# Kernel tuning notes

Measured on AMD Instinct MI355X. Metric: run time of the kernel, lower is better.

## Reference

```python
import jax, jax.numpy as jnp
import numpy as np

B = 16384
TEXT_D = 768
TECH_D = 256
IN_D = TEXT_D + TECH_D  # 1024
OUT_D = 1024
E = 8


def setup_inputs() -> dict:
    key = jax.random.key(0)
    ks = jax.random.split(key, 8)
    s_in = 1.0 / np.sqrt(IN_D)
    s_out = 1.0 / np.sqrt(OUT_D)
    return {
        "text_features": jax.random.normal(ks[0], (B, TEXT_D), jnp.float32),
        "technical_features": jax.random.normal(ks[1], (B, TECH_D), jnp.float32),
        # stacked expert params: layer1 [E, IN_D, OUT_D], layer2 [E, OUT_D, OUT_D]
        "W1": jax.random.uniform(ks[2], (E, IN_D, OUT_D), jnp.float32, -s_in, s_in),
        "b1": jax.random.uniform(ks[3], (E, OUT_D), jnp.float32, -s_in, s_in),
        "W2": jax.random.uniform(ks[4], (E, OUT_D, OUT_D), jnp.float32, -s_out, s_out),
        "b2": jax.random.uniform(ks[5], (E, OUT_D), jnp.float32, -s_out, s_out),
        # gating network
        "Wg": jax.random.uniform(ks[6], (IN_D, E), jnp.float32, -s_in, s_in),
        "bg": jax.random.uniform(ks[7], (E,), jnp.float32, -s_in, s_in),
    }


def reference(text_features, technical_features, W1, b1, W2, b2, Wg, bg):
    x = jnp.concatenate([text_features, technical_features], axis=-1)  # [B, IN_D]
    gates = jax.nn.softmax(x @ Wg + bg, axis=-1)                       # [B, E]
    h = jax.nn.relu(jnp.einsum('bi,eio->beo', x, W1) + b1[None])       # [B, E, OUT_D]
    y = jnp.einsum('beo,eop->bep', h, W2) + b2[None]                   # [B, E, OUT_D]
    return jnp.einsum('be,bep->bp', gates, y)                          # [B, OUT_D]
```

## Files before the change

kernel.cpp:

```cpp
#include <hip/hip_runtime.h>
#include <hip/hip_bf16.h>

#define NB 16384
#define TEXT_D 768
#define TECH_D 256
#define IND 1024
#define OUTD 1024
#define NE 8
#define KH2 4096

typedef unsigned short u16;
typedef __bf16 bf16x8 __attribute__((ext_vector_type(8)));
typedef float f32x4 __attribute__((ext_vector_type(4)));

__device__ __forceinline__ u16 f2bf(float f) {
  union { float f; unsigned int u; } x; x.f = f;
  unsigned int u = x.u;
  return (u16)((u + 0x7FFFu + ((u >> 16) & 1u)) >> 16);
}

__device__ __forceinline__ void gload_lds16(const void* g, void* l) {
  __builtin_amdgcn_global_load_lds(
      (const __attribute__((address_space(1))) unsigned int*)g,
      (__attribute__((address_space(3))) unsigned int*)l, 16, 0, 0);
}

__global__ __launch_bounds__(256) void convert_gates(
    const float* __restrict__ text, const float* __restrict__ tech,
    const float* __restrict__ Wg, const float* __restrict__ bg,
    u16* __restrict__ xb, float* __restrict__ gates) {
  int t = threadIdx.x;
  int wave = t >> 6, lane = t & 63;
  int row = blockIdx.x * 4 + wave;

  float acc[NE];
#pragma unroll
  for (int e = 0; e < NE; ++e) acc[e] = 0.f;

#pragma unroll
  for (int j = 0; j < 4; ++j) {
    int col = j * 256 + lane * 4;
    float4 v = (j < 3) ? *(const float4*)&text[(size_t)row * TEXT_D + col]
                       : *(const float4*)&tech[(size_t)row * TECH_D + lane * 4];
    ushort4 o = make_ushort4(f2bf(v.x), f2bf(v.y), f2bf(v.z), f2bf(v.w));
    *(ushort4*)&xb[(size_t)row * IND + col] = o;
    const float* wp = &Wg[(size_t)col * NE];
    float xv[4] = {v.x, v.y, v.z, v.w};
#pragma unroll
    for (int i = 0; i < 4; ++i) {
      float4 w0 = *(const float4*)&wp[i * NE];
      float4 w1 = *(const float4*)&wp[i * NE + 4];
      acc[0] = fmaf(xv[i], w0.x, acc[0]);
      acc[1] = fmaf(xv[i], w0.y, acc[1]);
      acc[2] = fmaf(xv[i], w0.z, acc[2]);
      acc[3] = fmaf(xv[i], w0.w, acc[3]);
      acc[4] = fmaf(xv[i], w1.x, acc[4]);
      acc[5] = fmaf(xv[i], w1.y, acc[5]);
      acc[6] = fmaf(xv[i], w1.z, acc[6]);
      acc[7] = fmaf(xv[i], w1.w, acc[7]);
    }
  }
#pragma unroll
  for (int off = 32; off; off >>= 1)
#pragma unroll
    for (int e = 0; e < NE; ++e) acc[e] += __shfl_xor(acc[e], off);

#pragma unroll
  for (int e = 0; e < NE; ++e) acc[e] += bg[e];
  float mx = acc[0];
#pragma unroll
  for (int e = 1; e < NE; ++e) mx = fmaxf(mx, acc[e]);
  float s = 0.f;
#pragma unroll
  for (int e = 0; e < NE; ++e) { acc[e] = expf(acc[e] - mx); s += acc[e]; }
  float inv = 1.f / s;
  if (lane < NE) gates[(size_t)row * NE + lane] = acc[lane] * inv;
}

__global__ __launch_bounds__(256) void transpose_w12(
    const float* __restrict__ W1, const float* __restrict__ W2,
    u16* __restrict__ W1t, u16* __restrict__ W2t) {
  __shared__ u16 tile[64][65];
  int bid = blockIdx.x;
  int half = bid >> 11;
  int b2 = bid & 2047;
  int e = b2 >> 8;
  int tb = b2 & 255;
  int r0 = (tb >> 4) * 64;
  int c0 = (tb & 15) * 64;
  const float* We; u16* Wte; int ostride;
  if (half == 0) {
    We = W1 + (size_t)e * IND * OUTD;
    Wte = W1t + ((size_t)e << 20);
    ostride = 1024;
  } else {
    We = W2 + (size_t)e * IND * OUTD;
    Wte = W2t + ((size_t)(e >> 2) << 22) + (size_t)(e & 3) * 1024;
    ostride = KH2;
  }
  int t = threadIdx.x;
  int tr = t >> 4;
  int tc = (t & 15) * 4;
#pragma unroll
  for (int j = 0; j < 4; ++j) {
    int row = j * 16 + tr;
    float4 v = *(const float4*)&We[(size_t)(r0 + row) * OUTD + c0 + tc];
    tile[row][tc + 0] = f2bf(v.x);
    tile[row][tc + 1] = f2bf(v.y);
    tile[row][tc + 2] = f2bf(v.z);
    tile[row][tc + 3] = f2bf(v.w);
  }
  __syncthreads();
#pragma unroll
  for (int j = 0; j < 4; ++j) {
    int row = j * 16 + tr;
    ushort4 o = make_ushort4(tile[tc + 0][row], tile[tc + 1][row],
                             tile[tc + 2][row], tile[tc + 3][row]);
    *(ushort4*)&Wte[(size_t)(c0 + row) * ostride + r0 + tc] = o;
  }
}

#define BAR() asm volatile("s_barrier" ::: "memory")
#define VM4() asm volatile("s_waitcnt vmcnt(4)" ::: "memory")

template <int SLOT, int K>
__device__ __forceinline__ void stage_slot(
    const u16* __restrict__ pA, const u16* __restrict__ pB, char* sb, int k0,
    int ch0, int rsub, int koff, int lbyte) {
#pragma unroll
  for (int j = 0; j < 2; ++j) {
    int ch = ch0 + j;
    int r;
    if constexpr (SLOT == 0)      r = (ch >> 3) * 128 + (ch & 7) * 8 + rsub;
    else if constexpr (SLOT == 3) r = 64 + (ch >> 3) * 128 + (ch & 7) * 8 + rsub;
    else if constexpr (SLOT == 1) r = (ch >> 2) * 64 + (ch & 3) * 8 + rsub;
    else                          r = (ch >> 2) * 64 + 32 + (ch & 3) * 8 + rsub;
    const u16* g = (SLOT == 0 || SLOT == 3) ? pA : pB;
    char* lb = sb + ((SLOT == 0 || SLOT == 3) ? 0 : 32768) + r * 128 + lbyte;
    gload_lds16(g + (size_t)r * K + k0 + koff, lb);
  }
}

template <int QH>
__device__ __forceinline__ void load_a(const char* rb, int wr, int lr, int hi,
                                       int swr, bf16x8 (&a)[4][2]) {
#pragma unroll
  for (int i = 0; i < 4; ++i)
#pragma unroll
    for (int ks = 0; ks < 2; ++ks)
      a[i][ks] = *(const bf16x8*)(rb + (wr * 128 + QH * 64 + i * 16 + lr) * 128
                                  + ((ks * 64 + hi * 16) ^ swr));
}

template <int NH>
__device__ __forceinline__ void load_b(const char* rb, int wc, int lr, int hi,
                                       int swr, bf16x8 (&b)[2][2]) {
#pragma unroll
  for (int q = 0; q < 2; ++q)
#pragma unroll
    for (int ks = 0; ks < 2; ++ks)
      b[q][ks] = *(const bf16x8*)(rb + 32768 +
                                  (wc * 64 + (NH * 2 + q) * 16 + lr) * 128
                                  + ((ks * 64 + hi * 16) ^ swr));
}

template <int MH, int NH>
__device__ __forceinline__ void mfma_quad(const bf16x8 (&a)[4][2],
                                          const bf16x8 (&b)[2][2],
                                          f32x4 (&acc)[8][4]) {
  __builtin_amdgcn_s_setprio(1);
#pragma unroll
  for (int i = 0; i < 4; ++i)
#pragma unroll
    for (int q = 0; q < 2; ++q) {
      acc[MH*4+i][NH*2+q] = __builtin_amdgcn_mfma_f32_16x16x32_bf16(
          a[i][0], b[q][0], acc[MH*4+i][NH*2+q], 0, 0, 0);
      acc[MH*4+i][NH*2+q] = __builtin_amdgcn_mfma_f32_16x16x32_bf16(
          a[i][1], b[q][1], acc[MH*4+i][NH*2+q], 0, 0, 0);
    }
  __builtin_amdgcn_s_setprio(0);
}

template <int RB, int K, bool LAST>
__device__ __forceinline__ void ktile(
    const u16* __restrict__ pA, const u16* __restrict__ pB, char* lds, int k0s,
    int ch0, int rsub, int koff, int lbyte,
    int wr, int wc, int lr, int hi, int swr,
    bf16x8 (&a)[4][2], bf16x8 (&b0)[2][2], bf16x8 (&b1)[2][2],
    f32x4 (&acc)[8][4]) {
  const char* rb = lds + RB * 65536;
  char* sb = lds + (RB ^ 1) * 65536;
  load_a<0>(rb, wr, lr, hi, swr, a);
  load_b<0>(rb, wc, lr, hi, swr, b0);
  if constexpr (!LAST) { stage_slot<0, K>(pA, pB, sb, k0s, ch0, rsub, koff, lbyte); VM4(); }
  else                 { asm volatile("s_waitcnt vmcnt(2)" ::: "memory"); }
  BAR();
  mfma_quad<0, 0>(a, b0, acc);
  BAR();
  load_b<1>(rb, wc, lr, hi, swr, b1);
  if constexpr (!LAST) { stage_slot<1, K>(pA, pB, sb, k0s, ch0, rsub, koff, lbyte); VM4(); }
  else                 { asm volatile("s_waitcnt vmcnt(0)" ::: "memory"); }
  BAR();
  mfma_quad<0, 1>(a, b1, acc);
  BAR();
  load_a<1>(rb, wr, lr, hi, swr, a);
  if constexpr (!LAST) { stage_slot<2, K>(pA, pB, sb, k0s, ch0, rsub, koff, lbyte); VM4(); }
  BAR();
  mfma_quad<1, 0>(a, b0, acc);
  BAR();
  if constexpr (!LAST) { stage_slot<3, K>(pA, pB, sb, k0s, ch0, rsub, koff, lbyte); VM4(); }
  BAR();
  mfma_quad<1, 1>(a, b1, acc);
  BAR();
}

template <int K>
__device__ __forceinline__ void core256(const u16* __restrict__ pA,
                                        const u16* __restrict__ pB,
                                        char* lds, int t, f32x4 (&acc)[8][4]) {
  constexpr int KT = K / 64;
  const int l = t & 63;
  const int w = t >> 6;
  const int wr = w >> 2, wc = w & 3;
  const int lr = l & 15, hi = l >> 4;
  const int rsub = l >> 3;
  const int koff = ((l & 7) ^ rsub) << 3;
  const int lbyte = (l & 7) * 16;
  const int ch0 = w * 2;
  const int swr = (lr & 7) << 4;

  bf16x8 a[4][2], b0[2][2], b1[2][2];

  stage_slot<0, K>(pA, pB, lds, 0, ch0, rsub, koff, lbyte);
  stage_slot<1, K>(pA, pB, lds, 0, ch0, rsub, koff, lbyte);
  stage_slot<2, K>(pA, pB, lds, 0, ch0, rsub, koff, lbyte);
  stage_slot<3, K>(pA, pB, lds, 0, ch0, rsub, koff, lbyte);
  VM4(); BAR();

  for (int T = 0; T < KT - 2; T += 2) {
    ktile<0, K, false>(pA, pB, lds, (T + 1) * 64, ch0, rsub, koff, lbyte,
                       wr, wc, lr, hi, swr, a, b0, b1, acc);
    ktile<1, K, false>(pA, pB, lds, (T + 2) * 64, ch0, rsub, koff, lbyte,
                       wr, wc, lr, hi, swr, a, b0, b1, acc);
  }
  ktile<0, K, false>(pA, pB, lds, (KT - 1) * 64, ch0, rsub, koff, lbyte,
                     wr, wc, lr, hi, swr, a, b0, b1, acc);
  ktile<1, K, true>(pA, pB, lds, 0, ch0, rsub, koff, lbyte,
                    wr, wc, lr, hi, swr, a, b0, b1, acc);
  asm volatile("s_waitcnt vmcnt(0)" ::: "memory");
}

__global__ __launch_bounds__(512, 2) void gemm1(
    const u16* __restrict__ xb, const u16* __restrict__ W1t,
    const float* __restrict__ b1, const float* __restrict__ gates,
    u16* __restrict__ Hg, int eg0) {
  __shared__ char lds[131072];
  int t = threadIdx.x;
  int nwg = gridDim.x, cpx = nwg >> 3, bid = blockIdx.x;
  int swz = (bid & 7) * cpx + (bid >> 3);
  int nb = swz & 3, ee = (swz >> 2) & 3, mb = swz >> 4;
  int e = eg0 + ee;

  f32x4 acc[8][4] = {};
  core256<1024>(xb + (size_t)mb * 256 * 1024,
                W1t + ((size_t)e << 20) + (size_t)nb * 256 * 1024,
                lds, t, acc);

  int l = t & 63, w = t >> 6, wr = w >> 2, wc = w & 3, lr = l & 15, hi = l >> 4;
  int m0 = mb * 256 + wr * 128 + hi * 4;
  int n0 = nb * 256 + wc * 64 + lr;
  const float* b1e = b1 + e * OUTD;
#pragma unroll
  for (int m = 0; m < 8; ++m) {
#pragma unroll
    for (int r = 0; r < 4; ++r) {
      int row = m0 + m * 16 + r;
      float g = gates[(size_t)row * NE + e];
#pragma unroll
      for (int nn = 0; nn < 4; ++nn) {
        int n = n0 + nn * 16;
        float v = g * fmaxf(acc[m][nn][r] + b1e[n], 0.f);
        Hg[(size_t)row * KH2 + ee * 1024 + n] = f2bf(v);
      }
    }
  }
}

template <bool FIRST>
__global__ __launch_bounds__(512, 2) void gemm2(
    const u16* __restrict__ Hg, const u16* __restrict__ W2th,
    const float* __restrict__ b2h, const float* __restrict__ gates,
    float* __restrict__ out, int eg0) {
  __shared__ char lds[131072];
  int t = threadIdx.x;
  int nwg = gridDim.x, cpx = nwg >> 3, bid = blockIdx.x;
  int swz = (bid & 7) * cpx + (bid >> 3);
  int nb = swz & 3, mb = swz >> 2;

  f32x4 acc[8][4] = {};
  core256<KH2>(Hg + (size_t)mb * 256 * KH2, W2th + (size_t)nb * 256 * KH2,
               lds, t, acc);

  int l = t & 63, w = t >> 6, wr = w >> 2, wc = w & 3, lr = l & 15, hi = l >> 4;
  int m0 = mb * 256 + wr * 128 + hi * 4;
  int n0 = nb * 256 + wc * 64 + lr;

  float bcol[4][4];
#pragma unroll
  for (int nn = 0; nn < 4; ++nn)
#pragma unroll
    for (int j = 0; j < 4; ++j)
      bcol[nn][j] = b2h[j * OUTD + n0 + nn * 16];

#pragma unroll
  for (int m = 0; m < 8; ++m) {
#pragma unroll
    for (int r = 0; r < 4; ++r) {
      int row = m0 + m * 16 + r;
      float4 ga = *(const float4*)&gates[(size_t)row * NE + eg0];
#pragma unroll
      for (int nn = 0; nn < 4; ++nn) {
        float bias = ga.x * bcol[nn][0] + ga.y * bcol[nn][1] +
                     ga.z * bcol[nn][2] + ga.w * bcol[nn][3];
        size_t oi = (size_t)row * OUTD + n0 + nn * 16;
        float v = acc[m][nn][r] + bias;
        if (FIRST) out[oi] = v;
        else       out[oi] += v;
      }
    }
  }
}

extern "C" void kernel_launch(void* const* d_in, const int* in_sizes, int n_in,
                              void* d_out, int out_size, void* d_ws, size_t ws_size,
                              hipStream_t stream) {
  (void)in_sizes; (void)n_in; (void)out_size; (void)ws_size;
  const float* text = (const float*)d_in[0];
  const float* tech = (const float*)d_in[1];
  const float* W1   = (const float*)d_in[2];
  const float* b1   = (const float*)d_in[3];
  const float* W2   = (const float*)d_in[4];
  const float* b2   = (const float*)d_in[5];
  const float* Wg   = (const float*)d_in[6];
  const float* bg   = (const float*)d_in[7];
  float* out = (float*)d_out;

  char* p = (char*)d_ws;
  u16* xb  = (u16*)p;  p += (size_t)NB * IND * 2;
  u16* W1t = (u16*)p;  p += (size_t)NE * IND * OUTD * 2;
  u16* W2t = (u16*)p;  p += (size_t)NE * OUTD * OUTD * 2;
  float* gates = (float*)p; p += (size_t)NB * NE * 4;
  u16* Hg  = (u16*)p;

  convert_gates<<<dim3(NB / 4), dim3(256), 0, stream>>>(text, tech, Wg, bg, xb, gates);
  transpose_w12<<<dim3(4096), dim3(256), 0, stream>>>(W1, W2, W1t, W2t);

  for (int h = 0; h < 2; ++h) {
    int eg0 = h * 4;
    gemm1<<<dim3(1024), dim3(512), 0, stream>>>(xb, W1t, b1, gates, Hg, eg0);
    const u16* W2th = W2t + ((size_t)h << 22);
    const float* b2h = b2 + (size_t)eg0 * OUTD;
    if (h == 0)
      gemm2<true><<<dim3(256), dim3(512), 0, stream>>>(Hg, W2th, b2h, gates, out, eg0);
    else
      gemm2<false><<<dim3(256), dim3(512), 0, stream>>>(Hg, W2th, b2h, gates, out, eg0);
  }
}
```

Measured before the change: 612.9 us.

## Deepen GEMM K-loop prefetch by staging half-tiles ahead into the current buffer

```diff
diff --git a/kernel.cpp b/kernel.cpp
--- a/kernel.cpp
+++ b/kernel.cpp
@@ -121,7 +121,9 @@
 }
 
 #define BAR() asm volatile("s_barrier" ::: "memory")
+#define VM0() asm volatile("s_waitcnt vmcnt(0)" ::: "memory")
 #define VM4() asm volatile("s_waitcnt vmcnt(4)" ::: "memory")
+#define VM8() asm volatile("s_waitcnt vmcnt(8)" ::: "memory")
 
 template <int SLOT, int K>
 __device__ __forceinline__ void stage_slot(
@@ -181,36 +183,42 @@
   __builtin_amdgcn_s_setprio(0);
 }
 
-template <int RB, int K, bool LAST>
+template <int RB, int K, int MODE>
 __device__ __forceinline__ void ktile(
-    const u16* __restrict__ pA, const u16* __restrict__ pB, char* lds, int k0s,
-    int ch0, int rsub, int koff, int lbyte,
+    const u16* __restrict__ pA, const u16* __restrict__ pB, char* lds,
+    int kH1, int kH0, int ch0, int rsub, int koff, int lbyte,
     int wr, int wc, int lr, int hi, int swr,
     bf16x8 (&a)[4][2], bf16x8 (&b0)[2][2], bf16x8 (&b1)[2][2],
     f32x4 (&acc)[8][4]) {
   const char* rb = lds + RB * 65536;
-  char* sb = lds + (RB ^ 1) * 65536;
+  char* nbuf = lds + (RB ^ 1) * 65536;
+  char* tbuf = lds + RB * 65536;
   load_a<0>(rb, wr, lr, hi, swr, a);
   load_b<0>(rb, wc, lr, hi, swr, b0);
-  if constexpr (!LAST) { stage_slot<0, K>(pA, pB, sb, k0s, ch0, rsub, koff, lbyte); VM4(); }
-  else                 { asm volatile("s_waitcnt vmcnt(2)" ::: "memory"); }
+  if constexpr (MODE < 2) {
+    stage_slot<2, K>(pA, pB, nbuf, kH1, ch0, rsub, koff, lbyte);
+    stage_slot<3, K>(pA, pB, nbuf, kH1, ch0, rsub, koff, lbyte);
+  }
   BAR();
   mfma_quad<0, 0>(a, b0, acc);
+  if constexpr (MODE == 2) { VM0(); } else { VM8(); }
   BAR();
   load_b<1>(rb, wc, lr, hi, swr, b1);
-  if constexpr (!LAST) { stage_slot<1, K>(pA, pB, sb, k0s, ch0, rsub, koff, lbyte); VM4(); }
-  else                 { asm volatile("s_waitcnt vmcnt(0)" ::: "memory"); }
   BAR();
   mfma_quad<0, 1>(a, b1, acc);
   BAR();
   load_a<1>(rb, wr, lr, hi, swr, a);
-  if constexpr (!LAST) { stage_slot<2, K>(pA, pB, sb, k0s, ch0, rsub, koff, lbyte); VM4(); }
   BAR();
   mfma_quad<1, 0>(a, b0, acc);
   BAR();
-  if constexpr (!LAST) { stage_slot<3, K>(pA, pB, sb, k0s, ch0, rsub, koff, lbyte); VM4(); }
+  if constexpr (MODE == 0) {
+    stage_slot<0, K>(pA, pB, tbuf, kH0, ch0, rsub, koff, lbyte);
+    stage_slot<1, K>(pA, pB, tbuf, kH0, ch0, rsub, koff, lbyte);
+  }
   BAR();
   mfma_quad<1, 1>(a, b1, acc);
+  if constexpr (MODE == 0) { VM8(); }
+  else if constexpr (MODE == 1) { VM4(); }
   BAR();
 }
 
@@ -219,6 +227,7 @@
                                         const u16* __restrict__ pB,
                                         char* lds, int t, f32x4 (&acc)[8][4]) {
   constexpr int KT = K / 64;
+  static_assert(KT >= 4 && (KT & 1) == 0, "KT must be even >= 4");
   const int l = t & 63;
   const int w = t >> 6;
   const int wr = w >> 2, wc = w & 3;
@@ -235,19 +244,21 @@
   stage_slot<1, K>(pA, pB, lds, 0, ch0, rsub, koff, lbyte);
   stage_slot<2, K>(pA, pB, lds, 0, ch0, rsub, koff, lbyte);
   stage_slot<3, K>(pA, pB, lds, 0, ch0, rsub, koff, lbyte);
-  VM4(); BAR();
+  stage_slot<0, K>(pA, pB, lds + 65536, 64, ch0, rsub, koff, lbyte);
+  stage_slot<1, K>(pA, pB, lds + 65536, 64, ch0, rsub, koff, lbyte);
+  VM8(); BAR();
 
   for (int T = 0; T < KT - 2; T += 2) {
-    ktile<0, K, false>(pA, pB, lds, (T + 1) * 64, ch0, rsub, koff, lbyte,
-                       wr, wc, lr, hi, swr, a, b0, b1, acc);
-    ktile<1, K, false>(pA, pB, lds, (T + 2) * 64, ch0, rsub, koff, lbyte,
-                       wr, wc, lr, hi, swr, a, b0, b1, acc);
-  }
-  ktile<0, K, false>(pA, pB, lds, (KT - 1) * 64, ch0, rsub, koff, lbyte,
-                     wr, wc, lr, hi, swr, a, b0, b1, acc);
-  ktile<1, K, true>(pA, pB, lds, 0, ch0, rsub, koff, lbyte,
-                    wr, wc, lr, hi, swr, a, b0, b1, acc);
-  asm volatile("s_waitcnt vmcnt(0)" ::: "memory");
+    ktile<0, K, 0>(pA, pB, lds, (T + 1) * 64, (T + 2) * 64, ch0, rsub, koff,
+                   lbyte, wr, wc, lr, hi, swr, a, b0, b1, acc);
+    ktile<1, K, 0>(pA, pB, lds, (T + 2) * 64, (T + 3) * 64, ch0, rsub, koff,
+                   lbyte, wr, wc, lr, hi, swr, a, b0, b1, acc);
+  }
+  ktile<0, K, 1>(pA, pB, lds, (KT - 1) * 64, 0, ch0, rsub, koff,
+                 lbyte, wr, wc, lr, hi, swr, a, b0, b1, acc);
+  ktile<1, K, 2>(pA, pB, lds, 0, 0, ch0, rsub, koff,
+                 lbyte, wr, wc, lr, hi, swr, a, b0, b1, acc);
+  VM0();
 }
 
 __global__ __launch_bounds__(512, 2) void gemm1(
```

After: 603.5 us. Within noise of the previous version (-1.5%).
